# Kernel tuning notes

Measured on AMD Instinct MI355X. Metric: run time of the kernel, lower is better.

Reference implementation:

```python
import jax, jax.numpy as jnp
import numpy as np

B, C, T = 524288, 10, 25

def setup_inputs() -> dict:
    key = jax.random.key(0)
    k1, k2, k3, k4 = jax.random.split(key, 4)
    mu = jax.random.normal(k1, (B, C), dtype=jnp.float32)
    log_sigma2 = jax.random.normal(k2, (B, C), dtype=jnp.float32)
    y = jax.random.randint(k3, (B,), 0, C, dtype=jnp.int64)
    # MVN(0, I) sample == iid standard normal noise, shape [T, B, C]
    eps = jax.random.normal(k4, (T, B, C), dtype=jnp.float32)
    return {"mu": mu, "log_sigma2": log_sigma2, "y": y, "eps": eps}

def reference(mu, log_sigma2, y, eps):
    T_ = eps.shape[0]
    # reparameterized logits: [T, B, C]
    logits = mu[None, :, :] + jnp.exp(0.5 * log_sigma2)[None, :, :] * eps
    # log_softmax over classes, minus log(T)
    logp = jax.nn.log_softmax(logits, axis=-1) - jnp.log(jnp.float32(T_))
    # logsumexp over the T MC samples -> [B, C]
    lse = jax.scipy.special.logsumexp(logp, axis=0)
    # nll_loss: mean of -log p(y)
    picked = jnp.take_along_axis(lse, y[:, None].astype(jnp.int32), axis=1)[:, 0]
    return -jnp.mean(picked)
```

## Files before the change

kernel.cpp:

```cpp
#include <hip/hip_runtime.h>
#include <math.h>

#define BB 524288
#define CC 10
#define TT 25
#define BLK 256
#define NBLK (BB / BLK)
#define WSLAB (64 * CC)
#define SLABF ((size_t)BB * CC)

#define GLL(src, dst, n)                                                    \
    __builtin_amdgcn_global_load_lds(                                       \
        (const __attribute__((address_space(1))) void*)(src),               \
        (__attribute__((address_space(3))) void*)(dst), n, 0, 0)

__global__ void init_out_kernel(float* out) {
    *out = logf((float)TT);
}

__global__ __launch_bounds__(256) void mc_nll_kernel(
    const float* __restrict__ mu,
    const float* __restrict__ ls2,
    const int*   __restrict__ y,
    const float* __restrict__ eps,
    float* __restrict__ out)
{
    __shared__ float slab[2][4][WSLAB];
    __shared__ float wsum[4];

    const int tid  = threadIdx.x;
    const int wid  = tid >> 6;
    const int lane = tid & 63;
    const int b    = blockIdx.x * BLK + tid;

    const int yi = y[b];

    float muv[CC], sig[CC];
    {
        const float2* m2 = reinterpret_cast<const float2*>(mu  + (size_t)b * CC);
        const float2* s2 = reinterpret_cast<const float2*>(ls2 + (size_t)b * CC);
#pragma unroll
        for (int i = 0; i < CC / 2; ++i) {
            float2 m = m2[i];
            float2 s = s2[i];
            muv[2 * i]     = m.x;
            muv[2 * i + 1] = m.y;
            sig[2 * i]     = __expf(0.5f * s.x);
            sig[2 * i + 1] = __expf(0.5f * s.y);
        }
    }

    const float* wbase = eps + (size_t)blockIdx.x * BLK * CC + wid * WSLAB;

    auto stage = [&](int t, int bf) {
        const float* s = wbase + (size_t)t * SLABF;
        float*       d = &slab[bf][wid][0];
        GLL(s + 4 * lane,        d,        16);
        GLL(s + 256 + 4 * lane,  d + 256,  16);
        GLL(s + 512 + lane,      d + 512,  4);
        GLL(s + 576 + lane,      d + 576,  4);
    };

    stage(0, 0);

    float S  = 0.0f;
    int   bf = 0;
    for (int t = 0; t < TT; ++t) {
        asm volatile("s_waitcnt lgkmcnt(0)" ::: "memory");
        if (t < TT - 1) {
            stage(t + 1, bf ^ 1);
            asm volatile("s_waitcnt vmcnt(4)" ::: "memory");
        } else {
            asm volatile("s_waitcnt vmcnt(0)" ::: "memory");
        }

        const float* row = &slab[bf][wid][lane * CC];
        float l[CC];
#pragma unroll
        for (int i = 0; i < CC / 2; ++i) {
            float2 e = *reinterpret_cast<const float2*>(row + 2 * i);
            l[2 * i]     = fmaf(sig[2 * i],     e.x, muv[2 * i]);
            l[2 * i + 1] = fmaf(sig[2 * i + 1], e.y, muv[2 * i + 1]);
        }
        float m = l[0];
#pragma unroll
        for (int c = 1; c < CC; ++c) m = fmaxf(m, l[c]);
        float s = 0.0f, ey = 0.0f;
#pragma unroll
        for (int c = 0; c < CC; ++c) {
            float x = __expf(l[c] - m);
            s += x;
            ey = (c == yi) ? x : ey;
        }
        S = fmaf(ey, __builtin_amdgcn_rcpf(s), S);
        bf ^= 1;
    }

    float x = __logf(S);
#pragma unroll
    for (int off = 32; off > 0; off >>= 1)
        x += __shfl_down(x, off, 64);

    if (lane == 0) wsum[wid] = x;
    __syncthreads();
    if (tid == 0) {
        float bs = wsum[0] + wsum[1] + wsum[2] + wsum[3];
        atomicAdd(out, -bs * (1.0f / (float)BB));
    }
}

extern "C" void kernel_launch(void* const* d_in, const int* in_sizes, int n_in,
                              void* d_out, int out_size, void* d_ws, size_t ws_size,
                              hipStream_t stream) {
    const float* mu  = (const float*)d_in[0];
    const float* ls2 = (const float*)d_in[1];
    const int*   y   = (const int*)d_in[2];
    const float* eps = (const float*)d_in[3];
    float* out = (float*)d_out;

    hipLaunchKernelGGL(init_out_kernel, dim3(1), dim3(1), 0, stream, out);
    hipLaunchKernelGGL(mc_nll_kernel, dim3(NBLK), dim3(BLK), 0, stream,
                       mu, ls2, y, eps, out);
}
```

Before: 109.9 us.

## Replace LDS-staged eps loads with direct nontemporal loads and two-pass reduction

Removes the double-buffered global_load_lds staging of eps through shared memory. Each thread now reads its own 10-float row directly with nontemporal 8-byte loads. The atomicAdd finalisation and the init kernel are replaced by per-block partial sums written to workspace, followed by a single-block reduce kernel. This avoids LDS traffic and waitcnt serialisation, but per-thread 40-byte-strided loads coalesce less well, and the change adds a second launch.

```diff
diff --git a/kernel.cpp b/kernel.cpp
--- a/kernel.cpp
+++ b/kernel.cpp
@@ -6,32 +6,18 @@
 #define TT 25
 #define BLK 256
 #define NBLK (BB / BLK)
-#define WSLAB (64 * CC)
 #define SLABF ((size_t)BB * CC)
 
-#define GLL(src, dst, n)                                                    \
-    __builtin_amdgcn_global_load_lds(                                       \
-        (const __attribute__((address_space(1))) void*)(src),               \
-        (__attribute__((address_space(3))) void*)(dst), n, 0, 0)
-
-__global__ void init_out_kernel(float* out) {
-    *out = logf((float)TT);
-}
+typedef float v2f __attribute__((ext_vector_type(2)));
 
 __global__ __launch_bounds__(256) void mc_nll_kernel(
     const float* __restrict__ mu,
     const float* __restrict__ ls2,
     const int*   __restrict__ y,
     const float* __restrict__ eps,
-    float* __restrict__ out)
+    float* __restrict__ ws)
 {
-    __shared__ float slab[2][4][WSLAB];
-    __shared__ float wsum[4];
-
-    const int tid  = threadIdx.x;
-    const int wid  = tid >> 6;
-    const int lane = tid & 63;
-    const int b    = blockIdx.x * BLK + tid;
+    const int b = blockIdx.x * BLK + threadIdx.x;
 
     const int yi = y[b];
 
@@ -50,35 +36,14 @@
         }
     }
 
-    const float* wbase = eps + (size_t)blockIdx.x * BLK * CC + wid * WSLAB;
-
-    auto stage = [&](int t, int bf) {
-        const float* s = wbase + (size_t)t * SLABF;
-        float*       d = &slab[bf][wid][0];
-        GLL(s + 4 * lane,        d,        16);
-        GLL(s + 256 + 4 * lane,  d + 256,  16);
-        GLL(s + 512 + lane,      d + 512,  4);
-        GLL(s + 576 + lane,      d + 576,  4);
-    };
-
-    stage(0, 0);
-
-    float S  = 0.0f;
-    int   bf = 0;
+    float S = 0.0f;
     for (int t = 0; t < TT; ++t) {
-        asm volatile("s_waitcnt lgkmcnt(0)" ::: "memory");
-        if (t < TT - 1) {
-            stage(t + 1, bf ^ 1);
-            asm volatile("s_waitcnt vmcnt(4)" ::: "memory");
-        } else {
-            asm volatile("s_waitcnt vmcnt(0)" ::: "memory");
-        }
-
-        const float* row = &slab[bf][wid][lane * CC];
+        const v2f* e2 = reinterpret_cast<const v2f*>(
+            eps + (size_t)t * SLABF + (size_t)b * CC);
         float l[CC];
 #pragma unroll
         for (int i = 0; i < CC / 2; ++i) {
-            float2 e = *reinterpret_cast<const float2*>(row + 2 * i);
+            v2f e = __builtin_nontemporal_load(e2 + i);
             l[2 * i]     = fmaf(sig[2 * i],     e.x, muv[2 * i]);
             l[2 * i + 1] = fmaf(sig[2 * i + 1], e.y, muv[2 * i + 1]);
         }
@@ -93,7 +58,6 @@
             ey = (c == yi) ? x : ey;
         }
         S = fmaf(ey, __builtin_amdgcn_rcpf(s), S);
-        bf ^= 1;
     }
 
     float x = __logf(S);
@@ -101,11 +65,35 @@
     for (int off = 32; off > 0; off >>= 1)
         x += __shfl_down(x, off, 64);
 
+    __shared__ float wsum[4];
+    const int lane = threadIdx.x & 63;
+    const int wid  = threadIdx.x >> 6;
+    if (lane == 0) wsum[wid] = x;
+    __syncthreads();
+    if (threadIdx.x == 0)
+        ws[blockIdx.x] = wsum[0] + wsum[1] + wsum[2] + wsum[3];
+}
+
+__global__ __launch_bounds__(256) void reduce_kernel(
+    const float* __restrict__ ws, float* __restrict__ out)
+{
+    const int tid = threadIdx.x;
+    float x = 0.0f;
+#pragma unroll
+    for (int j = 0; j < NBLK / 256; ++j)
+        x += ws[j * 256 + tid];
+#pragma unroll
+    for (int off = 32; off > 0; off >>= 1)
+        x += __shfl_down(x, off, 64);
+
+    __shared__ float wsum[4];
+    const int lane = tid & 63;
+    const int wid  = tid >> 6;
     if (lane == 0) wsum[wid] = x;
     __syncthreads();
     if (tid == 0) {
-        float bs = wsum[0] + wsum[1] + wsum[2] + wsum[3];
-        atomicAdd(out, -bs * (1.0f / (float)BB));
+        float total = wsum[0] + wsum[1] + wsum[2] + wsum[3];
+        *out = logf((float)TT) - total * (1.0f / (float)BB);
     }
 }
 
@@ -117,8 +105,9 @@
     const int*   y   = (const int*)d_in[2];
     const float* eps = (const float*)d_in[3];
     float* out = (float*)d_out;
+    float* ws  = (float*)d_ws;
 
-    hipLaunchKernelGGL(init_out_kernel, dim3(1), dim3(1), 0, stream, out);
     hipLaunchKernelGGL(mc_nll_kernel, dim3(NBLK), dim3(BLK), 0, stream,
-                       mu, ls2, y, eps, out);
+                       mu, ls2, y, eps, ws);
+    hipLaunchKernelGGL(reduce_kernel, dim3(1), dim3(BLK), 0, stream, ws, out);
 }
```

Measured after the change: 125.4 us. +14.1%, slower.
